# Performance work log

Measured on AMD Instinct MI355X. Metric: run time of the kernel, lower is better.

The kernel has to match this reference:

```python
import jax, jax.numpy as jnp
import numpy as np

GROUP = 256   # must equal 16*16 pooled positions for broadcast to work
K = 3         # unfold kernel size (hard-coded in original forward)
EPS = 1e-5    # BatchNorm eps


def setup_inputs() -> dict:
    key = jax.random.key(0)
    k1, k2 = jax.random.split(key, 2)
    n, c, h, w = 4, 256, 128, 128
    Ck = c // GROUP                      # = 1
    oc = Ck * K * K                      # = 9 (conv1 out channels)
    x = jax.random.normal(k1, (n, c, h, w), jnp.float32)
    w_conv = jax.random.normal(k2, (oc, c), jnp.float32) * 0.02  # 1x1 conv weight
    gamma = jnp.ones((oc,), jnp.float32)   # BN weight
    beta = jnp.zeros((oc,), jnp.float32)   # BN bias
    return {"x": x, "w_conv": w_conv, "gamma": gamma, "beta": beta}


def reference(x, w_conv, gamma, beta):
    n, c, h, w = x.shape
    Ck = c // GROUP
    kk = K * K
    # AdaptiveAvgPool2d((16,16)): h,w divisible by 16 -> uniform window average
    xp = x.reshape(n, c, 16, h // 16, 16, w // 16).mean(axis=(3, 5))  # (n,c,16,16)
    # 1x1 conv (no bias)
    sigma = jnp.einsum('oc,nchw->nohw', w_conv, xp)  # (n, Ck*9, 16, 16)
    # BatchNorm2d (training mode: batch statistics, biased variance)
    mu = sigma.mean(axis=(0, 2, 3), keepdims=True)
    var = sigma.var(axis=(0, 2, 3), keepdims=True)
    sigma = (sigma - mu) * jax.lax.rsqrt(var + EPS) \
        * gamma[None, :, None, None] + beta[None, :, None, None]
    # F.unfold(kernel_size=3, padding=1) -> (n, c, 9, h, w)
    xpad = jnp.pad(x, ((0, 0), (0, 0), (1, 1), (1, 1)))
    patches = jnp.stack(
        [xpad[:, :, i:i + h, j:j + w] for i in range(K) for j in range(K)],
        axis=2)  # (n, c, 9, h, w)
    # channel dim c splits contiguously into (GROUP, Ck)
    xg = patches.reshape(n, GROUP, Ck, kk, h * w)      # (n,256,Ck,9,hw)
    # sigma channel dim Ck*9 splits contiguously into (Ck, 9); spatial 16*16=256
    sg = sigma.reshape(n, Ck, kk, 16 * 16).transpose(0, 3, 1, 2)  # (n,256,Ck,9)
    # weighted sum over the 9 taps; group axis broadcasts against pooled-region axis
    out = jnp.einsum('ngkps,ngkp->ngks', xg, sg)       # (n,256,Ck,hw)
    return out.reshape(n, c, h, w)
```

## Files before the change

### kernel.cpp

```cpp
#include <hip/hip_runtime.h>

#define N_ 4
#define C_ 256
#define H_ 128
#define W_ 128
#define HW_ (H_*W_)
#define BINS 256
#define OC 9
#define EPS_ 1e-5f

__global__ __launch_bounds__(256) void pool_kernel(const float* __restrict__ x,
                                                   float* __restrict__ xp) {
    int b = blockIdx.x;
    int n = b >> 8, c = b & 255;
    const float4* xv = (const float4*)(x + (size_t)b * HW_);
    __shared__ float bins[BINS];
    int t = threadIdx.x;
    bins[t] = 0.f;
    __syncthreads();
    int xb = (t & 31) >> 1;
    #pragma unroll
    for (int k = 0; k < 16; ++k) {
        float4 v = xv[k * 256 + t];
        float s = v.x + v.y + v.z + v.w;
        atomicAdd(&bins[k * 16 + xb], s);
    }
    __syncthreads();
    xp[((size_t)n << 16) + (t << 8) + c] = bins[t] * (1.f / 64.f);
}

__global__ __launch_bounds__(64) void conv1x1_kernel(const float* __restrict__ xp,
                                                     const float* __restrict__ wconv,
                                                     float* __restrict__ sraw) {
    int b = blockIdx.x;
    int t = threadIdx.x;
    const float* xc = xp + ((size_t)b << 8);
    float v[4];
    #pragma unroll
    for (int i = 0; i < 4; ++i) v[i] = xc[i * 64 + t];
    #pragma unroll
    for (int o = 0; o < OC; ++o) {
        float s = 0.f;
        #pragma unroll
        for (int i = 0; i < 4; ++i) s += wconv[o * 256 + i * 64 + t] * v[i];
        #pragma unroll
        for (int off = 32; off > 0; off >>= 1) s += __shfl_down(s, off);
        if (t == 0) sraw[o * (N_ * BINS) + b] = s;
    }
}

__global__ __launch_bounds__(256) void bn_kernel(const float* __restrict__ sraw,
                                                 const float* __restrict__ gamma,
                                                 const float* __restrict__ beta,
                                                 float* __restrict__ w9) {
    int o = blockIdx.x;
    int t = threadIdx.x;
    const float* src = sraw + o * (N_ * BINS);
    float v[4], sum = 0.f, sq = 0.f;
    #pragma unroll
    for (int i = 0; i < 4; ++i) {
        v[i] = src[i * 256 + t];
        sum += v[i];
        sq += v[i] * v[i];
    }
    __shared__ float ls[8];
    __shared__ float sc[2];
    #pragma unroll
    for (int off = 32; off > 0; off >>= 1) {
        sum += __shfl_down(sum, off);
        sq  += __shfl_down(sq, off);
    }
    int wave = t >> 6;
    if ((t & 63) == 0) { ls[wave] = sum; ls[4 + wave] = sq; }
    __syncthreads();
    if (t == 0) {
        float S = ls[0] + ls[1] + ls[2] + ls[3];
        float Q = ls[4] + ls[5] + ls[6] + ls[7];
        float mu = S * (1.f / 1024.f);
        float var = Q * (1.f / 1024.f) - mu * mu;
        float scale = gamma[o] * rsqrtf(var + EPS_);
        sc[0] = scale;
        sc[1] = beta[o] - mu * scale;
    }
    __syncthreads();
    float scale = sc[0], shift = sc[1];
    #pragma unroll
    for (int i = 0; i < 4; ++i) {
        int idx = i * 256 + t;
        w9[idx * 9 + o] = v[i] * scale + shift;
    }
}

__global__ __launch_bounds__(256) void dwconv_kernel(const float* __restrict__ x,
                                                     const float* __restrict__ w9,
                                                     float* __restrict__ out) {
    int b = blockIdx.x;
    int plane = b >> 3;
    int rt = b & 7;
    int r0 = rt * 16;
    const float* xin = x + (size_t)plane * HW_;
    float* po = out + (size_t)plane * HW_;
    const float* wp = w9 + plane * 9;
    float w[9];
    #pragma unroll
    for (int i = 0; i < 9; ++i) w[i] = wp[i];

    __shared__ __align__(16) float lds[18 * 132];
    int t = threadIdx.x;
    if (t < 18) {
        lds[t * 132] = 0.f;
        lds[t * 132 + 129] = 0.f;
    }
    #pragma unroll
    for (int i = 0; i < 3; ++i) {
        int vi = i * 256 + t;
        if (vi < 576) {
            int lr = vi >> 5;
            int c4 = (vi & 31) << 2;
            int gr = r0 - 1 + lr;
            float4 val = make_float4(0.f, 0.f, 0.f, 0.f);
            if (gr >= 0 && gr < H_) val = *(const float4*)&xin[gr * W_ + c4];
            float* d = &lds[lr * 132 + c4 + 1];
            d[0] = val.x; d[1] = val.y; d[2] = val.z; d[3] = val.w;
        }
    }
    __syncthreads();

    int mr = t >> 5;
    int mc = t & 31;
    int olr = mr * 2;
    int oc0 = mc * 4;
    float rowv[4][6];
    #pragma unroll
    for (int j = 0; j < 4; ++j) {
        const float* rp = &lds[(olr + j) * 132 + oc0];
        float4 a = *(const float4*)rp;
        rowv[j][0] = a.x; rowv[j][1] = a.y; rowv[j][2] = a.z; rowv[j][3] = a.w;
        rowv[j][4] = rp[4]; rowv[j][5] = rp[5];
    }
    #pragma unroll
    for (int rr = 0; rr < 2; ++rr) {
        float res[4];
        #pragma unroll
        for (int cc = 0; cc < 4; ++cc) {
            float s = 0.f;
            #pragma unroll
            for (int dy = 0; dy < 3; ++dy)
                #pragma unroll
                for (int dx = 0; dx < 3; ++dx)
                    s += w[dy * 3 + dx] * rowv[rr + dy][cc + dx];
            res[cc] = s;
        }
        *(float4*)&po[(r0 + olr + rr) * W_ + oc0] =
            make_float4(res[0], res[1], res[2], res[3]);
    }
}

extern "C" void kernel_launch(void* const* d_in, const int* in_sizes, int n_in,
                              void* d_out, int out_size, void* d_ws, size_t ws_size,
                              hipStream_t stream) {
    const float* x     = (const float*)d_in[0];
    const float* wconv = (const float*)d_in[1];
    const float* gamma = (const float*)d_in[2];
    const float* beta  = (const float*)d_in[3];
    float* out = (float*)d_out;

    float* xp   = (float*)d_ws;
    float* sraw = xp + N_ * BINS * C_;
    float* w9   = sraw + OC * N_ * BINS;

    pool_kernel   <<<N_ * C_,      256, 0, stream>>>(x, xp);
    conv1x1_kernel<<<N_ * BINS,     64, 0, stream>>>(xp, wconv, sraw);
    bn_kernel     <<<OC,           256, 0, stream>>>(sraw, gamma, beta, w9);
    dwconv_kernel <<<N_ * C_ * 8,  256, 0, stream>>>(x, w9, out);
}
```

Before: 153.1 us.

## Fuse 1x1 conv with batchnorm and replace LDS atomics with shuffle reductions in pooling

The pooling kernel now reduces each row's pair of float4 sums with lane shuffles and writes per-wave partials to shared memory, replacing LDS atomicAdd. Its output is stored channel-major so that a single fused conv+BN kernel can compute the 1x1 conv and batch statistics together. This drops one launch and the intermediate sraw buffer. The trade-off is that the fused kernel runs on only 9 blocks, each looping serially over 256 channels, so the conv becomes a low-parallelism serial stage.

```diff
diff --git a/kernel.cpp b/kernel.cpp
--- a/kernel.cpp
+++ b/kernel.cpp
@@ -10,68 +10,57 @@
 #define EPS_ 1e-5f
 
 __global__ __launch_bounds__(256) void pool_kernel(const float* __restrict__ x,
-                                                   float* __restrict__ xp) {
+                                                   float* __restrict__ xpT) {
     int b = blockIdx.x;
     int n = b >> 8, c = b & 255;
     const float4* xv = (const float4*)(x + (size_t)b * HW_);
-    __shared__ float bins[BINS];
+    __shared__ float part[4 * 256];
     int t = threadIdx.x;
-    bins[t] = 0.f;
-    __syncthreads();
-    int xb = (t & 31) >> 1;
+    int w = t >> 6, l = t & 63;
+    int j = (l & 31) >> 1;
+    bool writer = (l < 32) && ((l & 1) == 0);
     #pragma unroll
     for (int k = 0; k < 16; ++k) {
         float4 v = xv[k * 256 + t];
         float s = v.x + v.y + v.z + v.w;
-        atomicAdd(&bins[k * 16 + xb], s);
+        s += __shfl_xor(s, 1);
+        s += __shfl_xor(s, 32);
+        if (writer) part[w * 256 + k * 16 + j] = s;
     }
     __syncthreads();
-    xp[((size_t)n << 16) + (t << 8) + c] = bins[t] * (1.f / 64.f);
+    float r = part[t] + part[256 + t] + part[512 + t] + part[768 + t];
+    xpT[((size_t)c << 10) + (n << 8) + t] = r * (1.f / 64.f);
 }
 
-__global__ __launch_bounds__(64) void conv1x1_kernel(const float* __restrict__ xp,
+__global__ __launch_bounds__(256) void convbn_kernel(const float* __restrict__ xpT,
                                                      const float* __restrict__ wconv,
-                                                     float* __restrict__ sraw) {
-    int b = blockIdx.x;
-    int t = threadIdx.x;
-    const float* xc = xp + ((size_t)b << 8);
-    float v[4];
-    #pragma unroll
-    for (int i = 0; i < 4; ++i) v[i] = xc[i * 64 + t];
-    #pragma unroll
-    for (int o = 0; o < OC; ++o) {
-        float s = 0.f;
-        #pragma unroll
-        for (int i = 0; i < 4; ++i) s += wconv[o * 256 + i * 64 + t] * v[i];
-        #pragma unroll
-        for (int off = 32; off > 0; off >>= 1) s += __shfl_down(s, off);
-        if (t == 0) sraw[o * (N_ * BINS) + b] = s;
-    }
-}
-
-__global__ __launch_bounds__(256) void bn_kernel(const float* __restrict__ sraw,
-                                                 const float* __restrict__ gamma,
-                                                 const float* __restrict__ beta,
-                                                 float* __restrict__ w9) {
+                                                     const float* __restrict__ gamma,
+                                                     const float* __restrict__ beta,
+                                                     float* __restrict__ w9) {
     int o = blockIdx.x;
     int t = threadIdx.x;
-    const float* src = sraw + o * (N_ * BINS);
-    float v[4], sum = 0.f, sq = 0.f;
-    #pragma unroll
-    for (int i = 0; i < 4; ++i) {
-        v[i] = src[i * 256 + t];
-        sum += v[i];
-        sq += v[i] * v[i];
+    const float* wrow = wconv + o * 256;
+    float acc0 = 0.f, acc1 = 0.f, acc2 = 0.f, acc3 = 0.f;
+    #pragma unroll 4
+    for (int c = 0; c < 256; ++c) {
+        float wv = wrow[c];
+        const float* p = xpT + (c << 10) + t;
+        acc0 += wv * p[0];
+        acc1 += wv * p[256];
+        acc2 += wv * p[512];
+        acc3 += wv * p[768];
     }
-    __shared__ float ls[8];
-    __shared__ float sc[2];
+    float sum = acc0 + acc1 + acc2 + acc3;
+    float sq  = acc0*acc0 + acc1*acc1 + acc2*acc2 + acc3*acc3;
     #pragma unroll
     for (int off = 32; off > 0; off >>= 1) {
         sum += __shfl_down(sum, off);
         sq  += __shfl_down(sq, off);
     }
-    int wave = t >> 6;
-    if ((t & 63) == 0) { ls[wave] = sum; ls[4 + wave] = sq; }
+    __shared__ float ls[8];
+    __shared__ float sc[2];
+    int w = t >> 6;
+    if ((t & 63) == 0) { ls[w] = sum; ls[4 + w] = sq; }
     __syncthreads();
     if (t == 0) {
         float S = ls[0] + ls[1] + ls[2] + ls[3];
@@ -84,11 +73,10 @@
     }
     __syncthreads();
     float scale = sc[0], shift = sc[1];
-    #pragma unroll
-    for (int i = 0; i < 4; ++i) {
-        int idx = i * 256 + t;
-        w9[idx * 9 + o] = v[i] * scale + shift;
-    }
+    w9[(0 * 256 + t) * 9 + o] = acc0 * scale + shift;
+    w9[(1 * 256 + t) * 9 + o] = acc1 * scale + shift;
+    w9[(2 * 256 + t) * 9 + o] = acc2 * scale + shift;
+    w9[(3 * 256 + t) * 9 + o] = acc3 * scale + shift;
 }
 
 __global__ __launch_bounds__(256) void dwconv_kernel(const float* __restrict__ x,
@@ -165,12 +153,10 @@
     const float* beta  = (const float*)d_in[3];
     float* out = (float*)d_out;
 
-    float* xp   = (float*)d_ws;
-    float* sraw = xp + N_ * BINS * C_;
-    float* w9   = sraw + OC * N_ * BINS;
+    float* xpT = (float*)d_ws;
+    float* w9  = xpT + C_ * N_ * BINS;
 
-    pool_kernel   <<<N_ * C_,      256, 0, stream>>>(x, xp);
-    conv1x1_kernel<<<N_ * BINS,     64, 0, stream>>>(xp, wconv, sraw);
-    bn_kernel     <<<OC,           256, 0, stream>>>(sraw, gamma, beta, w9);
-    dwconv_kernel <<<N_ * C_ * 8,  256, 0, stream>>>(x, w9, out);
+    pool_kernel  <<<N_ * C_,     256, 0, stream>>>(x, xpT);
+    convbn_kernel<<<OC,          256, 0, stream>>>(xpT, wconv, gamma, beta, w9);
+    dwconv_kernel<<<N_ * C_ * 8, 256, 0, stream>>>(x, w9, out);
 }
```

New measurement: 162.7 us. 6.2% more time.
